# Kernel tuning notes

Measured on AMD Instinct MI355X. Metric: run time of the kernel, lower is better.

Reference implementation:

```python
import jax, jax.numpy as jnp
import numpy as np

N, L, S, C, H = 8, 1024, 1024, 512, 8
SCALE = float((C // H) ** 0.5)  # sqrt(64), as in source (based on embed_dim, not cat'd dim)


def _linear_params(key, c_in, c_out):
    kw, kb = jax.random.split(key)
    lim = 1.0 / np.sqrt(c_in)
    W = jax.random.uniform(kw, (c_out, c_in), jnp.float32, -lim, lim)
    b = jax.random.uniform(kb, (c_out,), jnp.float32, -lim, lim)
    return W, b


def setup_inputs() -> dict:
    key = jax.random.key(0)
    ks = jax.random.split(key, 12)
    inp = {
        'q_c': jax.random.normal(ks[0], (N, L, C), jnp.float32),
        'q_p': jax.random.normal(ks[1], (N, L, C), jnp.float32),
        'k_c': jax.random.normal(ks[2], (N, S, C), jnp.float32),
        'k_p': jax.random.normal(ks[3], (N, S, C), jnp.float32),
        'v': jax.random.normal(ks[4], (N, S, C), jnp.float32),
        'attn_mask': jax.random.normal(ks[5], (N, H, L, S), jnp.float32),
    }
    for i, name in enumerate(['qc', 'qp', 'kc', 'kp', 'v', 'o']):
        W, b = _linear_params(ks[6 + i], C, C)
        inp[f'W_{name}'] = W
        inp[f'b_{name}'] = b
    return inp


def _split_head(x, h):
    n, l, c = x.shape
    return x.reshape(n, l, h, c // h).transpose(0, 2, 1, 3)  # (N,H,L,c/h)


def reference(q_c, q_p, k_c, k_p, v, attn_mask,
              W_qc, b_qc, W_qp, b_qp, W_kc, b_kc, W_kp, b_kp, W_v, b_v, W_o, b_o):
    # dual projections + cat -> (N, L, 2C)
    q = jnp.concatenate([q_c @ W_qc.T + b_qc, q_p @ W_qp.T + b_qp], axis=-1)
    k = jnp.concatenate([k_c @ W_kc.T + b_kc, k_p @ W_kp.T + b_kp], axis=-1)
    vv = v @ W_v.T + b_v
    q = _split_head(q, H)   # (N,H,L,2C/H)
    k = _split_head(k, H)   # (N,H,S,2C/H)
    vv = _split_head(vv, H)  # (N,H,S,C/H)
    attn = jnp.einsum('nhld,nhsd->nhls', q / SCALE, k) + attn_mask
    attn = jax.nn.softmax(attn, axis=-1)
    out = jnp.einsum('nhls,nhsd->nhld', attn, vv)
    out = out.transpose(0, 2, 1, 3).reshape(N, L, C)
    return out @ W_o.T + b_o
```

## Files before the change

kernel.cpp:

```cpp
#include <hip/hip_runtime.h>
#include <hip/hip_bf16.h>

typedef __bf16 bf16;
typedef __bf16 bf16x8 __attribute__((ext_vector_type(8)));
typedef float  f32x4  __attribute__((ext_vector_type(4)));
typedef float  f32x2  __attribute__((ext_vector_type(2)));

#define LOG2E        1.4426950408889634f
#define QSCALE_LOG2E 0.18033688011112043f
#define DEFER_THR    20.0f

#define GLDS(g, l)                                                        \
  __builtin_amdgcn_global_load_lds(                                       \
      (const __attribute__((address_space(1))) void*)(g),                 \
      (__attribute__((address_space(3))) void*)(l), 16, 0, 0)

#define VMCNT_BAR(n) do {                                                 \
  asm volatile("s_waitcnt vmcnt(" #n ")" ::: "memory");                   \
  __builtin_amdgcn_s_barrier();                                           \
  __builtin_amdgcn_sched_barrier(0);                                      \
} while (0)

__device__ __forceinline__ void stage_f32_tile(const float* __restrict__ src, int ld,
                                               char* dst, int tid) {
  #pragma unroll
  for (int t = 0; t < 8; ++t) {
    int c8  = tid + t * 256;
    int row = c8 >> 4;
    int h8  = c8 & 15;
    const f32x4 v = *reinterpret_cast<const f32x4*>(src + row * ld + h8 * 4);
    union { bf16 h[4]; unsigned long long u; } pk;
    pk.h[0] = (bf16)v[0]; pk.h[1] = (bf16)v[1];
    pk.h[2] = (bf16)v[2]; pk.h[3] = (bf16)v[3];
    int byte = (row << 7) + ((((h8 >> 1) ^ (row & 7)) << 4) | ((h8 & 1) << 3));
    *reinterpret_cast<unsigned long long*>(dst + byte) = pk.u;
  }
}

__device__ __forceinline__ void stage_bf16_tile(const bf16* __restrict__ src, int ld,
                                                char* dst, int tid) {
  #pragma unroll
  for (int t = 0; t < 4; ++t) {
    int c   = tid + t * 256;
    int row = c >> 3;
    int ck  = c & 7;
    const bf16x8 v = *reinterpret_cast<const bf16x8*>(src + row * ld + ck * 8);
    int byte = (row << 7) + (((ck ^ (row & 7)) << 4));
    *reinterpret_cast<bf16x8*>(dst + byte) = v;
  }
}

__global__ __launch_bounds__(256) void proj_gemm(
    const float* __restrict__ qc, const float* __restrict__ qp,
    const float* __restrict__ kc, const float* __restrict__ kp,
    const float* __restrict__ vin,
    const float* __restrict__ Wqc, const float* __restrict__ bqc,
    const float* __restrict__ Wqp, const float* __restrict__ bqp,
    const float* __restrict__ Wkc, const float* __restrict__ bkc,
    const float* __restrict__ Wkp, const float* __restrict__ bkp,
    const float* __restrict__ Wv,  const float* __restrict__ bv,
    bf16* __restrict__ Qws, bf16* __restrict__ Kws, bf16* __restrict__ Vtws) {
  __shared__ __align__(16) bf16 lA[128 * 64];
  __shared__ __align__(16) bf16 lB[128 * 64];
  char* lAb = (char*)lA;
  char* lBb = (char*)lB;

  const int bx = blockIdx.x;
  const int g  = bx >> 8;
  const int mt = (bx & 255) >> 2;
  const int nt = bx & 3;

  const float *A, *W, *bias;
  if      (g == 0) { A = qc;  W = Wqc; bias = bqc; }
  else if (g == 1) { A = qp;  W = Wqp; bias = bqp; }
  else if (g == 2) { A = kc;  W = Wkc; bias = bkc; }
  else if (g == 3) { A = kp;  W = Wkp; bias = bkp; }
  else             { A = vin; W = Wv;  bias = bv;  }

  const int tid  = threadIdx.x;
  const int lane = tid & 63, wid = tid >> 6;
  const int wr = wid >> 1, wc = wid & 1;
  const int lrow = lane & 15, lgrp = lane >> 4;

  const float* Abase = A + (size_t)(mt * 128) * 512;
  const float* Wbase = W + (size_t)(nt * 128) * 512;

  const f32x4 fz = {0.f, 0.f, 0.f, 0.f};
  f32x4 acc[4][4];
  #pragma unroll
  for (int i = 0; i < 4; ++i)
    #pragma unroll
    for (int j = 0; j < 4; ++j) acc[i][j] = fz;

  for (int k0 = 0; k0 < 512; k0 += 64) {
    __syncthreads();
    stage_f32_tile(Abase + k0, 512, lAb, tid);
    stage_f32_tile(Wbase + k0, 512, lBb, tid);
    __syncthreads();
    #pragma unroll
    for (int kk = 0; kk < 2; ++kk) {
      bf16x8 af[4], bfr[4];
      #pragma unroll
      for (int mf = 0; mf < 4; ++mf) {
        int row  = wr * 64 + mf * 16 + lrow;
        int byte = (row << 7) + ((((kk << 2) | lgrp) ^ (row & 7)) << 4);
        af[mf] = *reinterpret_cast<const bf16x8*>(lAb + byte);
      }
      #pragma unroll
      for (int nf = 0; nf < 4; ++nf) {
        int row  = wc * 64 + nf * 16 + lrow;
        int byte = (row << 7) + ((((kk << 2) | lgrp) ^ (row & 7)) << 4);
        bfr[nf] = *reinterpret_cast<const bf16x8*>(lBb + byte);
      }
      #pragma unroll
      for (int mf = 0; mf < 4; ++mf)
        #pragma unroll
        for (int nf = 0; nf < 4; ++nf)
          acc[mf][nf] = __builtin_amdgcn_mfma_f32_16x16x32_bf16(
              af[mf], bfr[nf], acc[mf][nf], 0, 0, 0);
    }
  }

  float bcol[4];
  #pragma unroll
  for (int nf = 0; nf < 4; ++nf)
    bcol[nf] = bias[nt * 128 + wc * 64 + nf * 16 + lrow];

  #pragma unroll
  for (int mf = 0; mf < 4; ++mf) {
    #pragma unroll
    for (int nf = 0; nf < 4; ++nf) {
      #pragma unroll
      for (int r = 0; r < 4; ++r) {
        int grow = mt * 128 + wr * 64 + mf * 16 + lgrp * 4 + r;
        int col  = nt * 128 + wc * 64 + nf * 16 + lrow;
        float vv = acc[mf][nf][r] + bcol[nf];
        bf16 hb  = (bf16)vv;
        int n = grow >> 10, tt = grow & 1023;
        if (g < 2) {
          int j = (g << 9) + col;
          Qws[(size_t)((((n << 3) + (j >> 7)) << 10) | tt) * 128 + (j & 127)] = hb;
        } else if (g < 4) {
          int j = ((g - 2) << 9) + col;
          Kws[(size_t)((((n << 3) + (j >> 7)) << 10) | tt) * 128 + (j & 127)] = hb;
        } else {
          int h = col >> 6, d = col & 63;
          Vtws[(size_t)((((n << 3) + h) << 6) + d) * 1024 + tt] = hb;
        }
      }
    }
  }
}

__global__ __launch_bounds__(256) void attn_fwd(
    const bf16* __restrict__ Qws, const bf16* __restrict__ Kws,
    const bf16* __restrict__ Vtws, const float* __restrict__ mask,
    bf16* __restrict__ Ows) {
  __shared__ __align__(16) char Kl[2][8192];
  __shared__ __align__(16) char Vl[2][4096];
  __shared__ __align__(16) char Ml[3][8192];
  __shared__ __align__(16) char Pl[4][1024];

  const int bx = blockIdx.x;
  const int nh = bx >> 4;
  const int qt = bx & 15;
  const int tid = threadIdx.x;
  const int lane = tid & 63, wid = tid >> 6;
  const int lrow = lane & 15, lgrp = lane >> 4;
  const int q0 = qt * 64 + wid * 16;

  const bf16* Qb = Qws + ((size_t)(nh * 1024 + q0 + lrow)) * 128 + lgrp * 8;
  bf16x8 qf[4];
  #pragma unroll
  for (int kk = 0; kk < 4; ++kk)
    qf[kk] = *reinterpret_cast<const bf16x8*>(Qb + kk * 32);

  const int kc0 = wid * 128 + lane;
  const int kr0 = kc0 >> 4, kd0 = kc0 & 15;
  const bf16* Kg0 = Kws + ((size_t)(nh * 1024 + kr0)) * 128 + (kd0 ^ ((kr0 >> 1) & 7)) * 8;
  const int kc1 = kc0 + 64;
  const int kr1 = kc1 >> 4, kd1 = kc1 & 15;
  const bf16* Kg1 = Kws + ((size_t)(nh * 1024 + kr1)) * 128 + (kd1 ^ ((kr1 >> 1) & 7)) * 8;
  const int vc  = wid * 64 + lane;
  const int vr  = vc >> 2, vs = vc & 3;
  const bf16* Vg = Vtws + ((size_t)(nh * 64 + vr)) * 1024 + vs * 8;
  const float* Mblk = mask + ((size_t)(nh * 1024) + qt * 64) * 1024;
  const int mc0 = wid * 64 + lane;
  const float* Mg0 = Mblk + (size_t)(mc0 >> 3) * 1024 + (mc0 & 7) * 4;
  const float* Mg1 = Mg0 + (size_t)32 * 1024;

  char* Pb = &Pl[wid][0];

  const f32x4 fz = {0.f, 0.f, 0.f, 0.f};
  f32x4 oacc[4];
  #pragma unroll
  for (int dt = 0; dt < 4; ++dt) oacc[dt] = fz;
  float m2[4], lsum[4];
  #pragma unroll
  for (int r = 0; r < 4; ++r) { m2[r] = 0.f; lsum[r] = 0.f; }

  auto stageKV = [&](char* Ksg, char* Vsg, int sN) {
    GLDS(Kg0 + (size_t)sN * 128, Ksg + wid * 2048);
    GLDS(Kg1 + (size_t)sN * 128, Ksg + wid * 2048 + 1024);
    GLDS(Vg + sN,                Vsg + wid * 1024);
  };
  auto stageM = [&](char* Msg, int sN) {
    GLDS(Mg0 + sN, Msg + wid * 1024);
    GLDS(Mg1 + sN, Msg + 4096 + wid * 1024);
  };

  auto compute = [&](const char* Kb, const char* Vb, const char* Mb) {
    bf16x8 kf0[4], kf1[4], vf[4];
    #pragma unroll
    for (int kk = 0; kk < 4; ++kk) {
      int cb = ((((kk << 2) | lgrp) ^ (lrow & 7)) << 4);
      kf0[kk] = *reinterpret_cast<const bf16x8*>(Kb + lrow * 512 + cb);
      kf1[kk] = *reinterpret_cast<const bf16x8*>(Kb + lrow * 512 + 256 + cb);
    }
    #pragma unroll
    for (int dt = 0; dt < 4; ++dt)
      vf[dt] = *reinterpret_cast<const bf16x8*>(Vb + (dt * 16 + lrow) * 64 + lgrp * 16);
    f32x2 mk[4];
    #pragma unroll
    for (int r = 0; r < 4; ++r) {
      int qrow = wid * 16 + lgrp * 4 + r;
      mk[r] = *reinterpret_cast<const f32x2*>(Mb + qrow * 128 + lrow * 8);
    }

    f32x4 sc0 = fz, sc1 = fz;
    __builtin_amdgcn_s_setprio(1);
    #pragma unroll
    for (int kk = 0; kk < 4; ++kk)
      sc0 = __builtin_amdgcn_mfma_f32_16x16x32_bf16(qf[kk], kf0[kk], sc0, 0, 0, 0);
    #pragma unroll
    for (int kk = 0; kk < 4; ++kk)
      sc1 = __builtin_amdgcn_mfma_f32_16x16x32_bf16(qf[kk], kf1[kk], sc1, 0, 0, 0);
    __builtin_amdgcn_s_setprio(0);

    float a0r[4], a1r[4];
    bool ok = true;
    #pragma unroll
    for (int r = 0; r < 4; ++r) {
      a0r[r] = fmaf(sc0[r], QSCALE_LOG2E, mk[r].x * LOG2E);
      a1r[r] = fmaf(sc1[r], QSCALE_LOG2E, mk[r].y * LOG2E);
      ok &= (fmaxf(a0r[r], a1r[r]) <= m2[r] + DEFER_THR);
    }
    if (__builtin_expect(!__all(ok), 0)) {
      #pragma unroll
      for (int r = 0; r < 4; ++r) {
        float tv = fmaxf(a0r[r], a1r[r]);
        tv = fmaxf(tv, __shfl_xor(tv, 1));
        tv = fmaxf(tv, __shfl_xor(tv, 2));
        tv = fmaxf(tv, __shfl_xor(tv, 4));
        tv = fmaxf(tv, __shfl_xor(tv, 8));
        float mn = fmaxf(m2[r], tv);
        float corr = exp2f(m2[r] - mn);
        m2[r] = mn;
        lsum[r] *= corr;
        #pragma unroll
        for (int dt = 0; dt < 4; ++dt) oacc[dt][r] *= corr;
      }
    }
    #pragma unroll
    for (int r = 0; r < 4; ++r) {
      float e0 = exp2f(a0r[r] - m2[r]);
      float e1 = exp2f(a1r[r] - m2[r]);
      lsum[r] += e0 + e1;
      union { bf16 h[2]; unsigned u; } pk;
      pk.h[0] = (bf16)e0; pk.h[1] = (bf16)e1;
      int row = lgrp * 4 + r;
      int byte = row * 64 + ((((lrow >> 2) ^ (row & 3)) << 4) | ((lrow & 3) << 2));
      *reinterpret_cast<unsigned*>(Pb + byte) = pk.u;
    }
    __builtin_amdgcn_wave_barrier();
    __builtin_amdgcn_sched_barrier(0);
    bf16x8 pf = *reinterpret_cast<const bf16x8*>(
        Pb + lrow * 64 + ((lgrp ^ (lrow & 3)) << 4));

    __builtin_amdgcn_s_setprio(1);
    #pragma unroll
    for (int dt = 0; dt < 4; ++dt)
      oacc[dt] = __builtin_amdgcn_mfma_f32_16x16x32_bf16(pf, vf[dt], oacc[dt], 0, 0, 0);
    __builtin_amdgcn_s_setprio(0);
  };

  char *kcur = &Kl[0][0], *knxt = &Kl[1][0];
  char *vcur = &Vl[0][0], *vnxt = &Vl[1][0];
  char *m0p = &Ml[0][0], *m1p = &Ml[1][0], *m2p = &Ml[2][0];

  stageM(m0p, 0);
  stageKV(kcur, vcur, 0);
  stageM(m1p, 32);
  VMCNT_BAR(2);

  for (int t = 0; t < 30; ++t) {
    stageKV(knxt, vnxt, (t + 1) * 32);
    stageM(m2p, (t + 2) * 32);
    compute(kcur, vcur, m0p);
    VMCNT_BAR(2);
    char* tp;
    tp = kcur; kcur = knxt; knxt = tp;
    tp = vcur; vcur = vnxt; vnxt = tp;
    tp = m0p; m0p = m1p; m1p = m2p; m2p = tp;
  }

  stageKV(knxt, vnxt, 31 * 32);
  compute(kcur, vcur, m0p);
  VMCNT_BAR(0);
  compute(knxt, vnxt, m1p);

  #pragma unroll
  for (int r = 0; r < 4; ++r) {
    float ss = lsum[r];
    ss += __shfl_xor(ss, 1);
    ss += __shfl_xor(ss, 2);
    ss += __shfl_xor(ss, 4);
    ss += __shfl_xor(ss, 8);
    lsum[r] = 1.0f / ss;
  }

  const int n = nh >> 3, h = nh & 7;
  bf16* Ob = Ows + ((size_t)(n * 1024 + q0 + lgrp * 4)) * 512 + h * 64 + lrow;
  #pragma unroll
  for (int dt = 0; dt < 4; ++dt)
    #pragma unroll
    for (int r = 0; r < 4; ++r)
      Ob[(size_t)r * 512 + dt * 16] = (bf16)(oacc[dt][r] * lsum[r]);
}

__global__ __launch_bounds__(256) void out_gemm(
    const bf16* __restrict__ Ows, const float* __restrict__ Wo,
    const float* __restrict__ bo, float* __restrict__ out) {
  __shared__ __align__(16) bf16 lA[128 * 64];
  __shared__ __align__(16) bf16 lB[128 * 64];
  char* lAb = (char*)lA;
  char* lBb = (char*)lB;

  const int bx = blockIdx.x;
  const int mt = bx >> 2;
  const int nt = bx & 3;
  const int tid = threadIdx.x;
  const int lane = tid & 63, wid = tid >> 6;
  const int wr = wid >> 1, wc = wid & 1;
  const int lrow = lane & 15, lgrp = lane >> 4;

  const bf16*  Abase = Ows + (size_t)(mt * 128) * 512;
  const float* Wbase = Wo  + (size_t)(nt * 128) * 512;

  const f32x4 fz = {0.f, 0.f, 0.f, 0.f};
  f32x4 acc[4][4];
  #pragma unroll
  for (int i = 0; i < 4; ++i)
    #pragma unroll
    for (int j = 0; j < 4; ++j) acc[i][j] = fz;

  for (int k0 = 0; k0 < 512; k0 += 64) {
    __syncthreads();
    stage_bf16_tile(Abase + k0, 512, lAb, tid);
    stage_f32_tile(Wbase + k0, 512, lBb, tid);
    __syncthreads();
    #pragma unroll
    for (int kk = 0; kk < 2; ++kk) {
      bf16x8 af[4], bfr[4];
      #pragma unroll
      for (int mf = 0; mf < 4; ++mf) {
        int row  = wr * 64 + mf * 16 + lrow;
        int byte = (row << 7) + ((((kk << 2) | lgrp) ^ (row & 7)) << 4);
        af[mf] = *reinterpret_cast<const bf16x8*>(lAb + byte);
      }
      #pragma unroll
      for (int nf = 0; nf < 4; ++nf) {
        int row  = wc * 64 + nf * 16 + lrow;
        int byte = (row << 7) + ((((kk << 2) | lgrp) ^ (row & 7)) << 4);
        bfr[nf] = *reinterpret_cast<const bf16x8*>(lBb + byte);
      }
      #pragma unroll
      for (int mf = 0; mf < 4; ++mf)
        #pragma unroll
        for (int nf = 0; nf < 4; ++nf)
          acc[mf][nf] = __builtin_amdgcn_mfma_f32_16x16x32_bf16(
              af[mf], bfr[nf], acc[mf][nf], 0, 0, 0);
    }
  }

  float bcol[4];
  #pragma unroll
  for (int nf = 0; nf < 4; ++nf)
    bcol[nf] = bo[nt * 128 + wc * 64 + nf * 16 + lrow];

  #pragma unroll
  for (int mf = 0; mf < 4; ++mf) {
    #pragma unroll
    for (int nf = 0; nf < 4; ++nf) {
      #pragma unroll
      for (int r = 0; r < 4; ++r) {
        int grow = mt * 128 + wr * 64 + mf * 16 + lgrp * 4 + r;
        int col  = nt * 128 + wc * 64 + nf * 16 + lrow;
        out[(size_t)grow * 512 + col] = acc[mf][nf][r] + bcol[nf];
      }
    }
  }
}

extern "C" void kernel_launch(void* const* d_in, const int* in_sizes, int n_in,
                              void* d_out, int out_size, void* d_ws, size_t ws_size,
                              hipStream_t stream) {
  const float* qc   = (const float*)d_in[0];
  const float* qp   = (const float*)d_in[1];
  const float* kc   = (const float*)d_in[2];
  const float* kp   = (const float*)d_in[3];
  const float* vin  = (const float*)d_in[4];
  const float* mask = (const float*)d_in[5];
  const float* Wqc  = (const float*)d_in[6];
  const float* bqc  = (const float*)d_in[7];
  const float* Wqp  = (const float*)d_in[8];
  const float* bqp  = (const float*)d_in[9];
  const float* Wkc  = (const float*)d_in[10];
  const float* bkc  = (const float*)d_in[11];
  const float* Wkp  = (const float*)d_in[12];
  const float* bkp  = (const float*)d_in[13];
  const float* Wv   = (const float*)d_in[14];
  const float* bv   = (const float*)d_in[15];
  const float* Wo   = (const float*)d_in[16];
  const float* bo   = (const float*)d_in[17];

  bf16* Qws  = (bf16*)d_ws;
  bf16* Kws  = Qws  + (size_t)8 * 1024 * 1024;
  bf16* Vtws = Kws  + (size_t)8 * 1024 * 1024;
  bf16* Ows  = Vtws + (size_t)4 * 1024 * 1024;

  proj_gemm<<<dim3(1280), dim3(256), 0, stream>>>(
      qc, qp, kc, kp, vin, Wqc, bqc, Wqp, bqp, Wkc, bkc, Wkp, bkp, Wv, bv,
      Qws, Kws, Vtws);
  attn_fwd<<<dim3(1024), dim3(256), 0, stream>>>(Qws, Kws, Vtws, mask, Ows);
  out_gemm<<<dim3(256), dim3(256), 0, stream>>>(Ows, Wo, bo, (float*)d_out);
}
```

Measured before the change: 199.8 us.

## Specialize waves for mask vs K/V loads and deepen mask prefetch pipeline

```diff
diff --git a/kernel.cpp b/kernel.cpp
--- a/kernel.cpp
+++ b/kernel.cpp
@@ -15,8 +15,8 @@
       (const __attribute__((address_space(1))) void*)(g),                 \
       (__attribute__((address_space(3))) void*)(l), 16, 0, 0)
 
-#define VMCNT_BAR(n) do {                                                 \
-  asm volatile("s_waitcnt vmcnt(" #n ")" ::: "memory");                   \
+#define WAITV(n) asm volatile("s_waitcnt vmcnt(" #n ")" ::: "memory")
+#define BARRIER() do {                                                    \
   __builtin_amdgcn_s_barrier();                                           \
   __builtin_amdgcn_sched_barrier(0);                                      \
 } while (0)
@@ -158,7 +158,7 @@
     bf16* __restrict__ Ows) {
   __shared__ __align__(16) char Kl[2][8192];
   __shared__ __align__(16) char Vl[2][4096];
-  __shared__ __align__(16) char Ml[3][8192];
+  __shared__ __align__(16) char Ml[5][8192];
   __shared__ __align__(16) char Pl[4][1024];
 
   const int bx = blockIdx.x;
@@ -175,19 +175,32 @@
   for (int kk = 0; kk < 4; ++kk)
     qf[kk] = *reinterpret_cast<const bf16x8*>(Qb + kk * 32);
 
-  const int kc0 = wid * 128 + lane;
-  const int kr0 = kc0 >> 4, kd0 = kc0 & 15;
-  const bf16* Kg0 = Kws + ((size_t)(nh * 1024 + kr0)) * 128 + (kd0 ^ ((kr0 >> 1) & 7)) * 8;
-  const int kc1 = kc0 + 64;
-  const int kr1 = kc1 >> 4, kd1 = kc1 & 15;
-  const bf16* Kg1 = Kws + ((size_t)(nh * 1024 + kr1)) * 128 + (kd1 ^ ((kr1 >> 1) & 7)) * 8;
-  const int vc  = wid * 64 + lane;
-  const int vr  = vc >> 2, vs = vc & 3;
-  const bf16* Vg = Vtws + ((size_t)(nh * 64 + vr)) * 1024 + vs * 8;
   const float* Mblk = mask + ((size_t)(nh * 1024) + qt * 64) * 1024;
-  const int mc0 = wid * 64 + lane;
-  const float* Mg0 = Mblk + (size_t)(mc0 >> 3) * 1024 + (mc0 & 7) * 4;
-  const float* Mg1 = Mg0 + (size_t)32 * 1024;
+  const float* Mg = Mblk + (size_t)(lane >> 3) * 1024 +
+                    (((lane & 7) ^ (lane >> 3)) << 2);
+
+  const bf16* sgp[4];
+  char* sdp[4];
+  int srcMul = 128, dstStride = 8192;
+  if (wid == 1 || wid == 2) {
+    #pragma unroll
+    for (int jj = 0; jj < 4; ++jj) {
+      int j = (wid - 1) * 4 + jj;
+      int c = j * 64 + lane;
+      int key = c >> 4, kd = c & 15;
+      sgp[jj] = Kws + ((size_t)(nh * 1024 + key)) * 128 + (kd ^ ((key >> 1) & 7)) * 8;
+      sdp[jj] = (char*)&Kl[0][0] + j * 1024;
+    }
+  } else if (wid == 3) {
+    #pragma unroll
+    for (int jj = 0; jj < 4; ++jj) {
+      int c = jj * 64 + lane;
+      int vr = c >> 2, vs = c & 3;
+      sgp[jj] = Vtws + ((size_t)(nh * 64 + vr)) * 1024 + vs * 8;
+      sdp[jj] = (char*)&Vl[0][0] + jj * 1024;
+    }
+    srcMul = 1; dstStride = 4096;
+  }
 
   char* Pb = &Pl[wid][0];
 
@@ -199,14 +212,17 @@
   #pragma unroll
   for (int r = 0; r < 4; ++r) { m2[r] = 0.f; lsum[r] = 0.f; }
 
-  auto stageKV = [&](char* Ksg, char* Vsg, int sN) {
-    GLDS(Kg0 + (size_t)sN * 128, Ksg + wid * 2048);
-    GLDS(Kg1 + (size_t)sN * 128, Ksg + wid * 2048 + 1024);
-    GLDS(Vg + sN,                Vsg + wid * 1024);
+  auto stageM = [&](char* dst, int sN) {
+    #pragma unroll
+    for (int i = 0; i < 8; ++i)
+      GLDS(Mg + i * 8192 + sN, dst + i * 1024);
   };
-  auto stageM = [&](char* Msg, int sN) {
-    GLDS(Mg0 + sN, Msg + wid * 1024);
-    GLDS(Mg1 + sN, Msg + 4096 + wid * 1024);
+  auto stageKV = [&](int buf, int sN) {
+    if (wid >= 1) {
+      #pragma unroll
+      for (int jj = 0; jj < 4; ++jj)
+        GLDS(sgp[jj] + (size_t)sN * srcMul, sdp[jj] + buf * dstStride);
+    }
   };
 
   auto compute = [&](const char* Kb, const char* Vb, const char* Mb) {
@@ -224,7 +240,9 @@
     #pragma unroll
     for (int r = 0; r < 4; ++r) {
       int qrow = wid * 16 + lgrp * 4 + r;
-      mk[r] = *reinterpret_cast<const f32x2*>(Mb + qrow * 128 + lrow * 8);
+      int mchunk = (lrow >> 1) ^ (qrow & 7);
+      mk[r] = *reinterpret_cast<const f32x2*>(
+          Mb + qrow * 128 + (mchunk << 4) + ((lrow & 1) << 3));
     }
 
     f32x4 sc0 = fz, sc1 = fz;
@@ -284,30 +302,44 @@
     __builtin_amdgcn_s_setprio(0);
   };
 
-  char *kcur = &Kl[0][0], *knxt = &Kl[1][0];
-  char *vcur = &Vl[0][0], *vnxt = &Vl[1][0];
-  char *m0p = &Ml[0][0], *m1p = &Ml[1][0], *m2p = &Ml[2][0];
-
-  stageM(m0p, 0);
-  stageKV(kcur, vcur, 0);
-  stageM(m1p, 32);
-  VMCNT_BAR(2);
-
-  for (int t = 0; t < 30; ++t) {
-    stageKV(knxt, vnxt, (t + 1) * 32);
-    stageM(m2p, (t + 2) * 32);
-    compute(kcur, vcur, m0p);
-    VMCNT_BAR(2);
-    char* tp;
-    tp = kcur; kcur = knxt; knxt = tp;
-    tp = vcur; vcur = vnxt; vnxt = tp;
-    tp = m0p; m0p = m1p; m1p = m2p; m2p = tp;
-  }
-
-  stageKV(knxt, vnxt, 31 * 32);
-  compute(kcur, vcur, m0p);
-  VMCNT_BAR(0);
-  compute(knxt, vnxt, m1p);
+  char *mr0 = &Ml[0][0], *mr1 = &Ml[1][0], *mr2 = &Ml[2][0],
+       *mr3 = &Ml[3][0], *mr4 = &Ml[4][0];
+  auto rotM = [&]() {
+    char* tp = mr0; mr0 = mr1; mr1 = mr2; mr2 = mr3; mr3 = mr4; mr4 = tp;
+  };
+
+  if (wid == 0) {
+    stageM(mr0, 0); stageM(mr1, 32); stageM(mr2, 64); stageM(mr3, 96);
+  } else {
+    stageKV(0, 0);
+  }
+  if (wid == 0) { WAITV(24); } else { WAITV(0); }
+  BARRIER();
+
+  for (int t = 0; t < 28; ++t) {
+    if (wid == 0) stageM(mr4, (t + 4) * 32);
+    else          stageKV((t + 1) & 1, (t + 1) * 32);
+    compute(&Kl[t & 1][0], &Vl[t & 1][0], mr0);
+    if (wid == 0) { WAITV(24); } else { WAITV(0); }
+    BARRIER();
+    rotM();
+  }
+  stageKV(1, 29 * 32);
+  compute(&Kl[0][0], &Vl[0][0], mr0);
+  if (wid == 0) { WAITV(16); } else { WAITV(0); }
+  BARRIER(); rotM();
+
+  stageKV(0, 30 * 32);
+  compute(&Kl[1][0], &Vl[1][0], mr0);
+  if (wid == 0) { WAITV(8); } else { WAITV(0); }
+  BARRIER(); rotM();
+
+  stageKV(1, 31 * 32);
+  compute(&Kl[0][0], &Vl[0][0], mr0);
+  WAITV(0);
+  BARRIER(); rotM();
+
+  compute(&Kl[1][0], &Vl[1][0], mr0);
 
   #pragma unroll
   for (int r = 0; r < 4; ++r) {
```

New measurement: 198.7 us. About the same (-0.5%).
